# Performance work log

Hardware: AMD Instinct MI355X
Metric: run time of the kernel (lower is better)

## Reference

```python
import jax, jax.numpy as jnp
import numpy as np

NUM_EMBEDDINGS = 4096
EMBEDDING_DIM = 256
COMMITMENT_COST = 0.25
N_INPUTS = 65536


def setup_inputs() -> dict:
    key = jax.random.key(0)
    k1, k2 = jax.random.split(key)
    inputs = jax.random.normal(k1, (N_INPUTS, EMBEDDING_DIM), dtype=jnp.float32)
    lim = 1.0 / NUM_EMBEDDINGS
    codebook = jax.random.uniform(k2, (NUM_EMBEDDINGS, EMBEDDING_DIM),
                                  dtype=jnp.float32, minval=-lim, maxval=lim)
    return {"inputs": inputs, "codebook": codebook}


def reference(inputs, codebook):
    distances = (jnp.sum(inputs ** 2, axis=1, keepdims=True)
                 + jnp.sum(codebook ** 2, axis=1)
                 - 2.0 * jnp.matmul(inputs, codebook.T))
    encoding_indices = jnp.argmin(distances, axis=1)              # [N]
    quantized = codebook[encoding_indices]                        # gather == one_hot @ codebook

    e_latent_loss = jnp.mean((inputs - jax.lax.stop_gradient(quantized)) ** 2)
    q_latent_loss = jnp.mean((quantized - jax.lax.stop_gradient(inputs)) ** 2)
    loss = q_latent_loss + COMMITMENT_COST * e_latent_loss

    quantized_st = inputs + jax.lax.stop_gradient(quantized - inputs)

    # avg one-hot probs == normalized code counts
    counts = jnp.bincount(encoding_indices, length=NUM_EMBEDDINGS)
    avg_probs = counts.astype(jnp.float32) / inputs.shape[0]
    perplexity = jnp.exp(-jnp.sum(avg_probs * jnp.log(avg_probs + 1e-10)))

    return quantized_st, loss, perplexity, encoding_indices
```

## Files before the change

### kernel.cpp

```cpp
#include <hip/hip_runtime.h>
#include <hip/hip_bf16.h>
#include <math.h>

#define N_INPUTS 65536
#define NUM_EMB 4096
#define DIM 256
#define TAU_H 9.0e-4f
#define CAP 120
#define QSC 1.0e6f
#define WLCAP 1536

#define OFF_B    0
#define OFF_CAND 49152
#define OFF_RMIN 79872
#define OFF_CNT  80128
#define OFF_NX2  80384
#define OFF_WLC  80640
#define LDS_SZ   80704
#define OFF_WL   0
#define OFF_X    12288
#define OFF_BST  78848
#define OFF_BIX  79104
#define OFF_RED  0

typedef __attribute__((ext_vector_type(8))) short bf16x8;
typedef __attribute__((ext_vector_type(4))) float f32x4;

__device__ __forceinline__ unsigned enc32(float f) {
    unsigned u = __float_as_uint(f);
    return (u & 0x80000000u) ? ~u : (u | 0x80000000u);
}
__device__ __forceinline__ float dec32(unsigned e) {
    unsigned u = (e & 0x80000000u) ? (e & 0x7FFFFFFFu) : ~e;
    return __uint_as_float(u);
}
__device__ __forceinline__ unsigned short f2bf_rne(float f) {
    unsigned u = __float_as_uint(f);
    return (unsigned short)((u + 0x7FFFu + ((u >> 16) & 1u)) >> 16);
}

__device__ __forceinline__ float pw128_sq(const float* __restrict__ a) {
    float r[8];
    #pragma unroll
    for (int j = 0; j < 8; ++j) r[j] = __fmul_rn(a[j], a[j]);
    #pragma unroll
    for (int i = 8; i < 128; i += 8)
        #pragma unroll
        for (int j = 0; j < 8; ++j)
            r[j] = __fadd_rn(r[j], __fmul_rn(a[i + j], a[i + j]));
    return __fadd_rn(__fadd_rn(__fadd_rn(r[0], r[1]), __fadd_rn(r[2], r[3])),
                     __fadd_rn(__fadd_rn(r[4], r[5]), __fadd_rn(r[6], r[7])));
}
__device__ __forceinline__ float pw256_sq(const float* __restrict__ a) {
    return __fadd_rn(pw128_sq(a), pw128_sq(a + 128));
}

__global__ __launch_bounds__(256) void prep_cb(
        const float* __restrict__ src, float* __restrict__ norms,
        char* dst_base) {
    __shared__ float xs[64 * 260];
    const int t = threadIdx.x, b = blockIdx.x;
    const size_t rowbase = (size_t)b * 64;
    const float4* g = (const float4*)(src + rowbase * DIM);
    float4* s4 = (float4*)xs;
    #pragma unroll
    for (int k = 0; k < 16; ++k) {
        int p = t + k * 256, r = p >> 6, c = p & 63;
        s4[r * 65 + c] = g[p];
    }
    __syncthreads();
    if (t < 64) norms[rowbase + t] = pw256_sq(xs + t * 260);
    #pragma unroll
    for (int k = 0; k < 16; ++k) {
        int p = t + k * 256, r = p >> 6, c = p & 63;
        float4 v = s4[r * 65 + c];
        ushort4 u;
        u.x = f2bf_rne(v.x); u.y = f2bf_rne(v.y);
        u.z = f2bf_rne(v.z); u.w = f2bf_rne(v.w);
        ((ushort4*)(dst_base + (rowbase + r) * 1024 + 384))[c] = u;
    }
}

__device__ float exact_score(const float* xr, const float* __restrict__ er,
                             float nx2r, float ne2v) {
    float a = 0.f;
    for (int d = 0; d < DIM; d += 16) {
        float4 xa = *(const float4*)(xr + d);
        float4 xb = *(const float4*)(xr + d + 4);
        float4 xc = *(const float4*)(xr + d + 8);
        float4 xd = *(const float4*)(xr + d + 12);
        float4 e0 = *(const float4*)(er + d);
        float4 e1 = *(const float4*)(er + d + 4);
        float4 e2 = *(const float4*)(er + d + 8);
        float4 e3 = *(const float4*)(er + d + 12);
        a = fmaf(xa.x, e0.x, a); a = fmaf(xa.y, e0.y, a);
        a = fmaf(xa.z, e0.z, a); a = fmaf(xa.w, e0.w, a);
        a = fmaf(xb.x, e1.x, a); a = fmaf(xb.y, e1.y, a);
        a = fmaf(xb.z, e1.z, a); a = fmaf(xb.w, e1.w, a);
        a = fmaf(xc.x, e2.x, a); a = fmaf(xc.y, e2.y, a);
        a = fmaf(xc.z, e2.z, a); a = fmaf(xc.w, e2.w, a);
        a = fmaf(xd.x, e3.x, a); a = fmaf(xd.y, e3.y, a);
        a = fmaf(xd.z, e3.z, a); a = fmaf(xd.w, e3.w, a);
    }
    float t1 = __fadd_rn(nx2r, ne2v);
    return __fsub_rn(t1, __fmul_rn(2.f, a));
}

__global__ __launch_bounds__(256, 2) void gemm_fused(
        const float* __restrict__ x,
        const char* cbB,
        const float* __restrict__ cb,
        const float* __restrict__ ne2,
        float* outp,
        float* __restrict__ outidx,
        int* __restrict__ counts, float* __restrict__ partials) {
    __shared__ __align__(16) char L[LDS_SZ];

    const int tid = threadIdx.x;
    const int w = tid >> 6, lane = tid & 63;
    const int wr = w >> 1, wc = w & 1;
    const size_t brow = (size_t)blockIdx.x * 64;
    const bool writeq = (blockIdx.x >= NUM_EMB / 64);
    const int srcoff = ((lane & 7) ^ (lane >> 3)) << 4;

    unsigned* rminp = (unsigned*)(L + OFF_RMIN);
    unsigned* cntp  = (unsigned*)(L + OFF_CNT);
    float*    nx2l  = (float*)(L + OFF_NX2);
    unsigned* wlcnt = (unsigned*)(L + OFF_WLC);
    unsigned (*cand)[CAP] = (unsigned (*)[CAP])(L + OFF_CAND);

    if (tid < 64) { rminp[tid] = 0xFFFFFFFFu; cntp[tid] = 0u; }
    if (tid == 64) *wlcnt = 0u;

    bf16x8 af[2][8];
    float* xs = (float*)L;
    #pragma unroll
    for (int h = 0; h < 2; ++h) {
        const float4* g = (const float4*)(x + (brow + (size_t)h * 32) * DIM);
        #pragma unroll
        for (int r = 0; r < 8; ++r) {
            int p = tid + r * 256, rr = p >> 6, c = p & 63;
            ((float4*)xs)[rr * 65 + c] = g[p];
        }
        __syncthreads();
        if (tid < 32) nx2l[h * 32 + tid] = pw256_sq(xs + tid * 260);
        if (wr == h) {
            #pragma unroll
            for (int m = 0; m < 2; ++m) {
                #pragma unroll
                for (int ks = 0; ks < 8; ++ks) {
                    const float* rp = xs + (m * 16 + (lane & 15)) * 260
                                      + ks * 32 + (lane >> 4) * 8;
                    float4 a = *(const float4*)rp, b = *(const float4*)(rp + 4);
                    bf16x8 v;
                    v[0] = (short)f2bf_rne(a.x); v[1] = (short)f2bf_rne(a.y);
                    v[2] = (short)f2bf_rne(a.z); v[3] = (short)f2bf_rne(a.w);
                    v[4] = (short)f2bf_rne(b.x); v[5] = (short)f2bf_rne(b.y);
                    v[6] = (short)f2bf_rne(b.z); v[7] = (short)f2bf_rne(b.w);
                    af[m][ks] = v;
                }
            }
        }
        __syncthreads();
    }

    auto stageB = [&](int buf, int ct, int tt) {
        #pragma unroll
        for (int i = 0; i < 4; ++i) {
            int chunk = w * 4 + i;
            int code = ct * 128 + chunk * 8 + (lane >> 3);
            const char* gb = cbB + (size_t)code * 1024 + tt * 128 + srcoff;
            __builtin_amdgcn_global_load_lds(
                (const __attribute__((address_space(1))) unsigned*)gb,
                (__attribute__((address_space(3))) unsigned*)(L + buf * 16384 + chunk * 1024),
                16, 0, 0);
        }
    };

    f32x4 acc[2][4];
    #pragma unroll
    for (int m = 0; m < 2; ++m)
        #pragma unroll
        for (int n = 0; n < 4; ++n) acc[m][n] = (f32x4){0.f, 0.f, 0.f, 0.f};

    int cur = 0, nxt = 1;
    stageB(0, 0, 0);

    #pragma unroll 4
    for (int s = 0; s < 128; ++s) {
        const int tt = s & 3;
        float ne2h[4];
        if (tt == 3) {
            const int ct = s >> 2;
            #pragma unroll
            for (int n = 0; n < 4; ++n)
                ne2h[n] = 0.5f * ne2[ct * 128 + wc * 64 + n * 16 + (lane & 15)];
        }
        if (s < 127) {
            const int s1 = s + 1;
            stageB(nxt, s1 >> 2, s1 & 3);
        }
        if (s < 127) asm volatile("s_waitcnt vmcnt(4)" ::: "memory");
        else         asm volatile("s_waitcnt vmcnt(0)" ::: "memory");
        __builtin_amdgcn_s_barrier();
        __builtin_amdgcn_sched_barrier(0);

        #pragma unroll
        for (int kk = 0; kk < 2; ++kk) {
            bf16x8 bg[4];
            #pragma unroll
            for (int n = 0; n < 4; ++n) {
                int cc = wc * 64 + n * 16 + (lane & 15);
                int g = (kk * 4 + (lane >> 4)) ^ (cc & 7);
                bg[n] = *(const bf16x8*)(L + cur * 16384 + cc * 128 + (g << 4));
            }
            #pragma unroll
            for (int m = 0; m < 2; ++m)
                #pragma unroll
                for (int n = 0; n < 4; ++n)
                    acc[m][n] = __builtin_amdgcn_mfma_f32_16x16x32_bf16(
                        af[m][tt * 2 + kk], bg[n], acc[m][n], 0, 0, 0);
        }

        if (tt == 3) {
            const int ct = s >> 2;
            #pragma unroll
            for (int m = 0; m < 2; ++m) {
                #pragma unroll
                for (int j = 0; j < 4; ++j) {
                    float v = fminf(fminf(ne2h[0] - acc[m][0][j], ne2h[1] - acc[m][1][j]),
                                    fminf(ne2h[2] - acc[m][2][j], ne2h[3] - acc[m][3][j]));
                    #pragma unroll
                    for (int off = 1; off < 16; off <<= 1)
                        v = fminf(v, __shfl_xor(v, off, 64));
                    const int rowl = wr * 32 + m * 16 + (lane >> 4) * 4 + j;
                    if ((lane & 15) == 0) atomicMin(&rminp[rowl], enc32(v));
                    float th = fminf(dec32(rminp[rowl]), v) + TAU_H;
                    #pragma unroll
                    for (int n = 0; n < 4; ++n) {
                        float sc = ne2h[n] - acc[m][n][j];
                        if (sc <= th) {
                            int col = ct * 128 + wc * 64 + n * 16 + (lane & 15);
                            int q = (int)rintf(sc * QSC) + 32768;
                            q = max(0, min(65535, q));
                            unsigned pos = atomicAdd(&cntp[rowl], 1u);
                            if (pos < CAP)
                                cand[rowl][pos] = ((unsigned)q << 16) | (unsigned)col;
                        }
                    }
                    acc[m][0][j] = 0.f; acc[m][1][j] = 0.f;
                    acc[m][2][j] = 0.f; acc[m][3][j] = 0.f;
                }
            }
        }
        cur = nxt; nxt = (nxt + 1 == 3) ? 0 : nxt + 1;
    }
    __syncthreads();

    unsigned long long* wl = (unsigned long long*)(L + OFF_WL);
    if (tid < 64) {
        unsigned c = cntp[tid];
        if (c <= CAP) {
            float mav = dec32(rminp[tid]);
            int qthr = (int)rintf((mav + TAU_H) * QSC) + 1 + 32768;
            for (unsigned p = 0; p < c; ++p) {
                unsigned e = cand[tid][p];
                if ((int)(e >> 16) <= qthr) {
                    unsigned pos = atomicAdd(wlcnt, 1u);
                    if (pos < WLCAP)
                        wl[pos] = (unsigned long long)((tid << 16) | (e & 0xFFFFu));
                    else cntp[tid] = CAP + 1000u;
                }
            }
        }
    }
    __syncthreads();

    float* xl = (float*)(L + OFF_X);
    {
        const float4* g = (const float4*)(x + brow * DIM);
        #pragma unroll
        for (int k = 0; k < 16; ++k) {
            int p = tid + k * 256, gr = p >> 6, gc = p & 63;
            ((float4*)xl)[gr * 65 + gc] = g[p];
        }
    }
    unsigned* bst = (unsigned*)(L + OFF_BST);
    unsigned* bix = (unsigned*)(L + OFF_BIX);
    if (tid < 64) bst[tid] = 0xFFFFFFFFu;
    else if (tid < 128) bix[tid - 64] = 0xFFFFFFFFu;
    __syncthreads();

    const unsigned wn0 = *wlcnt;
    const unsigned wn = wn0 < WLCAP ? wn0 : WLCAP;
    for (unsigned i = tid; i < wn; i += 256) {
        unsigned lo = (unsigned)wl[i];
        int row = lo >> 16, code = lo & 0xFFFFu;
        float sv = exact_score(xl + row * 260, cb + (size_t)code * DIM,
                               nx2l[row], ne2[code]);
        wl[i] = ((unsigned long long)enc32(sv) << 32) | lo;
        atomicMin(&bst[row], enc32(sv));
    }
    for (int r = w; r < 64; r += 4) {
        if (cntp[r] > CAP) {
            float nr = nx2l[r];
            const float* xr = xl + r * 260;
            for (int c = lane; c < NUM_EMB; c += 64) {
                float sv = exact_score(xr, cb + (size_t)c * DIM, nr, ne2[c]);
                atomicMin(&bst[r], enc32(sv));
            }
        }
    }
    __syncthreads();

    for (unsigned i = tid; i < wn; i += 256) {
        unsigned long long v = wl[i];
        unsigned lo = (unsigned)v;
        int row = lo >> 16;
        if ((unsigned)(v >> 32) == bst[row])
            atomicMin(&bix[row], lo & 0xFFFFu);
    }
    for (int r = w; r < 64; r += 4) {
        if (cntp[r] > CAP) {
            float nr = nx2l[r];
            const float* xr = xl + r * 260;
            for (int c = lane; c < NUM_EMB; c += 64) {
                float sv = exact_score(xr, cb + (size_t)c * DIM, nr, ne2[c]);
                if (enc32(sv) == bst[r]) atomicMin(&bix[r], (unsigned)c);
            }
        }
    }
    __syncthreads();

    {
        const int r = tid >> 2, c0 = (tid & 3) * 16;
        int idx = (int)bix[r];
        idx = max(0, min(NUM_EMB - 1, idx));
        const float4* crq = (const float4*)(cb + (size_t)idx * DIM);
        const float4* xr4 = (const float4*)(xl + r * 260);
        float ss = 0.f;
        float4* oq = (float4*)(outp + (brow + r) * DIM);
        #pragma unroll
        for (int k = 0; k < 16; ++k) {
            float4 q = crq[c0 + k], xv = xr4[c0 + k];
            if (writeq) oq[c0 + k] = q;
            float dx = xv.x - q.x, dy = xv.y - q.y, dz = xv.z - q.z, dw = xv.w - q.w;
            ss += dx * dx + dy * dy + dz * dz + dw * dw;
        }
        if ((tid & 3) == 0) {
            outidx[brow + r] = (float)idx;
            atomicAdd(&counts[idx], 1);
        }
        float* red = (float*)(L + OFF_RED);
        red[tid] = ss;
        __syncthreads();
        for (int st2 = 128; st2; st2 >>= 1) {
            if (tid < st2) red[tid] += red[tid + st2];
            __syncthreads();
        }
        if (tid == 0) partials[blockIdx.x] = red[0];
    }
}

__global__ __launch_bounds__(256) void fixup_q(
        const float* __restrict__ cb, const float* __restrict__ outidx,
        float* __restrict__ outp) {
    const int t = threadIdx.x, b = blockIdx.x;
    const size_t row = (size_t)b * 64 + (t >> 2);
    const int c0 = (t & 3) * 16;
    int idx = (int)outidx[row];
    idx = max(0, min(NUM_EMB - 1, idx));
    const float4* crq = (const float4*)(cb + (size_t)idx * DIM);
    float4* oq = (float4*)(outp + row * DIM);
    #pragma unroll
    for (int k = 0; k < 16; ++k) oq[c0 + k] = crq[c0 + k];
}

__global__ void finalize_kernel(const float* __restrict__ partials, int np,
                                const int* __restrict__ counts,
                                float* __restrict__ out_loss,
                                float* __restrict__ out_perp) {
    __shared__ double sh[256];
    const int t = threadIdx.x;
    double s = 0.0;
    for (int i = t; i < np; i += 256) s += (double)partials[i];
    sh[t] = s; __syncthreads();
    for (int st = 128; st; st >>= 1) { if (t < st) sh[t] += sh[t + st]; __syncthreads(); }
    double sse = sh[0];
    __syncthreads();
    double h = 0.0;
    for (int k = t; k < NUM_EMB; k += 256) {
        double p = (double)counts[k] / (double)N_INPUTS;
        h -= p * log(p + 1e-10);
    }
    sh[t] = h; __syncthreads();
    for (int st = 128; st; st >>= 1) { if (t < st) sh[t] += sh[t + st]; __syncthreads(); }
    if (t == 0) {
        double mse = sse / ((double)N_INPUTS * (double)DIM);
        out_loss[0] = (float)(1.25 * mse);
        out_perp[0] = (float)exp(sh[0]);
    }
}

extern "C" void kernel_launch(void* const* d_in, const int* in_sizes, int n_in,
                              void* d_out, int out_size, void* d_ws, size_t ws_size,
                              hipStream_t stream) {
    const float* x  = (const float*)d_in[0];
    const float* cb = (const float*)d_in[1];
    float* out      = (float*)d_out;

    float* out_q    = out;
    float* out_loss = out + (size_t)N_INPUTS * DIM;
    float* out_perp = out_loss + 1;
    float* out_idx  = out_perp + 1;

    float* ne2      = (float*)d_ws;
    int*   counts   = (int*)((char*)d_ws + 16384);
    float* partials = (float*)((char*)d_ws + 32768);

    hipMemsetAsync(counts, 0, NUM_EMB * sizeof(int), stream);

    prep_cb<<<NUM_EMB / 64, 256, 0, stream>>>(cb, ne2, (char*)out);

    gemm_fused<<<N_INPUTS / 64, 256, 0, stream>>>(
        x, (const char*)out + 384, cb, ne2, out, out_idx, counts, partials);

    fixup_q<<<NUM_EMB / 64, 256, 0, stream>>>(cb, out_idx, out);

    finalize_kernel<<<1, 256, 0, stream>>>(partials, N_INPUTS / 64, counts,
                                           out_loss, out_perp);
}
```

Measured before the change: 415.3 us.

## Deepen codebook LDS pipeline to prefetch two stages ahead with early fragment reads

Changes the triple-buffered codebook staging from one-ahead to two-ahead prefetch, prologue-loading two stages. All B fragments for the stage are read from LDS before the next global-to-LDS issue and barrier, and the MFMA block is wrapped in s_setprio to favor matrix issue. The aim is to hide global load latency and LDS read latency behind MFMA work. In exchange it needs more registers for the eight held fragments. The barrier placement around buffer reuse also needs care to avoid overwriting a buffer still being read.

```diff
diff --git a/kernel.cpp b/kernel.cpp
--- a/kernel.cpp
+++ b/kernel.cpp
@@ -183,12 +183,26 @@
         #pragma unroll
         for (int n = 0; n < 4; ++n) acc[m][n] = (f32x4){0.f, 0.f, 0.f, 0.f};
 
-    int cur = 0, nxt = 1;
+    int cur = 0;
     stageB(0, 0, 0);
+    stageB(1, 0, 1);
+    asm volatile("s_waitcnt vmcnt(4)" ::: "memory");
+    __syncthreads();
 
     #pragma unroll 4
     for (int s = 0; s < 128; ++s) {
         const int tt = s & 3;
+
+        bf16x8 bg[2][4];
+        #pragma unroll
+        for (int kk = 0; kk < 2; ++kk)
+            #pragma unroll
+            for (int n = 0; n < 4; ++n) {
+                int cc = wc * 64 + n * 16 + (lane & 15);
+                int g = (kk * 4 + (lane >> 4)) ^ (cc & 7);
+                bg[kk][n] = *(const bf16x8*)(L + cur * 16384 + cc * 128 + (g << 4));
+            }
+
         float ne2h[4];
         if (tt == 3) {
             const int ct = s >> 2;
@@ -196,31 +210,28 @@
             for (int n = 0; n < 4; ++n)
                 ne2h[n] = 0.5f * ne2[ct * 128 + wc * 64 + n * 16 + (lane & 15)];
         }
-        if (s < 127) {
-            const int s1 = s + 1;
-            stageB(nxt, s1 >> 2, s1 & 3);
-        }
-        if (s < 127) asm volatile("s_waitcnt vmcnt(4)" ::: "memory");
-        else         asm volatile("s_waitcnt vmcnt(0)" ::: "memory");
+
+        if (s < 126) {
+            const int s2 = s + 2;
+            int tgt = cur + 2; if (tgt >= 3) tgt -= 3;
+            stageB(tgt, s2 >> 2, s2 & 3);
+            asm volatile("s_waitcnt vmcnt(4)" ::: "memory");
+        } else {
+            asm volatile("s_waitcnt vmcnt(0)" ::: "memory");
+        }
         __builtin_amdgcn_s_barrier();
         __builtin_amdgcn_sched_barrier(0);
 
-        #pragma unroll
-        for (int kk = 0; kk < 2; ++kk) {
-            bf16x8 bg[4];
-            #pragma unroll
-            for (int n = 0; n < 4; ++n) {
-                int cc = wc * 64 + n * 16 + (lane & 15);
-                int g = (kk * 4 + (lane >> 4)) ^ (cc & 7);
-                bg[n] = *(const bf16x8*)(L + cur * 16384 + cc * 128 + (g << 4));
-            }
+        __builtin_amdgcn_s_setprio(1);
+        #pragma unroll
+        for (int kk = 0; kk < 2; ++kk)
             #pragma unroll
             for (int m = 0; m < 2; ++m)
                 #pragma unroll
                 for (int n = 0; n < 4; ++n)
                     acc[m][n] = __builtin_amdgcn_mfma_f32_16x16x32_bf16(
-                        af[m][tt * 2 + kk], bg[n], acc[m][n], 0, 0, 0);
-        }
+                        af[m][tt * 2 + kk], bg[kk][n], acc[m][n], 0, 0, 0);
+        __builtin_amdgcn_s_setprio(0);
 
         if (tt == 3) {
             const int ct = s >> 2;
@@ -253,7 +264,7 @@
                 }
             }
         }
-        cur = nxt; nxt = (nxt + 1 == 3) ? 0 : nxt + 1;
+        cur = (cur + 1 == 3) ? 0 : cur + 1;
     }
     __syncthreads();
 
```

New measurement: 415.4 us. Within noise of the previous version (+0.0%).
